# Optimization experiments

Hardware: AMD Instinct MI355X
Metric: run time of the kernel (lower is better)

The kernel has to match this reference:

```python
import jax, jax.numpy as jnp
import numpy as np

N_SERIES = 32768
N_TIME = 512
SEAS = 24
MAX_NUM_SERIES = 32768
OUTPUT_SIZE = 7


def setup_inputs() -> dict:
    key = jax.random.key(0)
    k1, k2, k3, k4, k5 = jax.random.split(key, 5)
    # y must be strictly positive (divisions and logs of levels)
    y = jax.random.uniform(k1, (N_SERIES, N_TIME), jnp.float32) + 0.5
    idxs = jax.random.randint(k2, (N_SERIES,), 0, MAX_NUM_SERIES)
    lev_sms = jax.random.normal(k3, (MAX_NUM_SERIES, 1), jnp.float32) * 0.5
    seas_sms = jax.random.normal(k4, (MAX_NUM_SERIES, 1), jnp.float32) * 0.5
    init_seas = jax.random.normal(k5, (MAX_NUM_SERIES, SEAS), jnp.float32) * 0.1
    return {
        "y": y,
        "idxs": idxs,
        "lev_sms": lev_sms,
        "seas_sms": seas_sms,
        "init_seas": init_seas,
        "seasonality": SEAS,
        "output_size": OUTPUT_SIZE,
    }


def _es_forward(y, idxs, lev_sms_p, seas_sms_p, init_seas_p, seasonality, output_size):
    n_series, n_time = y.shape
    lev_sms = jax.nn.sigmoid(lev_sms_p[idxs, 0])          # (n,)
    # NOTE: faithful to original code, which (buggy or not) derives seas_sms
    # from self.lev_sms as well; seas_sms_p is an unused parameter.
    seas_sms = jax.nn.sigmoid(lev_sms_p[idxs, 0])         # (n,)
    init_seas = jnp.exp(init_seas_p[idxs, :])             # (n, seasonality)

    lev0 = y[:, 0] / init_seas[:, 0]                      # levels[:,0]

    # Ring-buffer formulation of the lag-`seasonality` recurrence:
    # original reads seasonalities[:, t] and writes seasonalities[:, t+seasonality];
    # both map to slot t % seasonality (read-before-write). Initial buffer slots
    # equal init_seas columns (slot 0 = init_seas[:,0], which also covers the
    # duplicated entry seasonalities[:, seasonality]).
    positions = jnp.arange(1, n_time) % seasonality       # (n_time-1,)
    y_steps = y[:, 1:].T                                  # (n_time-1, n)

    def step(carry, xs):
        lev_prev, buf = carry                             # (n,), (n, seasonality)
        y_t, pos = xs
        seas_t = buf[:, pos]
        newlev = lev_sms * (y_t / seas_t) + (1.0 - lev_sms) * lev_prev
        newseason = seas_sms * (y_t / newlev) + (1.0 - seas_sms) * seas_t
        log_diff = jnp.log(newlev) - jnp.log(lev_prev)
        buf = buf.at[:, pos].set(newseason)
        return (newlev, buf), (newlev, newseason, log_diff)

    _, (levs, seasons, logd) = jax.lax.scan(step, (lev0, init_seas), (y_steps, positions))

    levels = jnp.concatenate([lev0[:, None], levs.T], axis=1)              # (n, n_time)
    seasonalities = jnp.concatenate(
        [init_seas, init_seas[:, :1], seasons.T], axis=1                   # (n, seasonality+n_time)
    )
    log_diff_of_levels = logd.T                                            # (n, n_time-1)

    if output_size > seasonality:
        # faithful to original (which uses len(seasonalities) == n_series)
        start = seasonalities.shape[0] - seasonality
        end = start + output_size - seasonality
        seasonalities = jnp.concatenate([seasonalities, seasonalities[:, start:end]], axis=1)

    return levels, seasonalities, log_diff_of_levels


def reference(y, idxs, lev_sms, seas_sms, init_seas, seasonality, output_size):
    return _es_forward(y, idxs, lev_sms, seas_sms, init_seas, seasonality, output_size)
```

## Files before the change

### kernel.cpp

```cpp
#include <hip/hip_runtime.h>

#define NT 512
#define SEASN 24

constexpr int SEA_STRIDE = NT + SEASN;
constexpr int LOG_STRIDE = NT - 1;
constexpr float LN2 = 0.6931471805599453f;

constexpr int YS = 65;
constexpr int TS = 33;

__device__ __forceinline__ float frcp(float x)  { return __builtin_amdgcn_rcpf(x); }
__device__ __forceinline__ float flog2(float x) { return __builtin_amdgcn_logf(x); }

__device__ __forceinline__ void gl_lds4(const float* g, float* lds) {
    __builtin_amdgcn_global_load_lds(
        (const __attribute__((address_space(1))) void*)g,
        (__attribute__((address_space(3))) void*)lds, 4, 0, 0);
}

template<int PHASE, bool FIRST>
__device__ __forceinline__ void compute_subtile(const float* __restrict__ yb,
                                                float* __restrict__ lt,
                                                float* __restrict__ st,
                                                float lsm, float (&buf)[SEASN],
                                                float& lev)
{
    float yp[32];
    #pragma unroll
    for (int k = 0; k < 32; ++k) yp[k] = yb[k];
    #pragma unroll
    for (int k = 0; k < 32; ++k) {
        const int pos = (PHASE + k) % SEASN;
        const float yt = yp[k];
        if (FIRST && k == 0) {
            lev = yt * frcp(buf[0]);
            lt[0] = lev;
            st[0] = buf[0];
        } else {
            const float sv = buf[pos];
            const float nl = lev + lsm * (yt * frcp(sv) - lev);
            const float ns = sv + lsm * (yt * frcp(nl) - sv);
            lt[k] = nl; st[k] = ns;
            lev = nl; buf[pos] = ns;
        }
    }
}

__device__ __forceinline__ void flush_sub(const float* __restrict__ lt,
                                          const float* __restrict__ st,
                                          int sf, int q, int rr, int sbase,
                                          float* __restrict__ levels,
                                          float* __restrict__ seasv,
                                          float* __restrict__ logd)
{
    const int tb = sf * 32;
    #pragma unroll
    for (int i = 0; i < 8; ++i) {
        const int r = 8 * i + rr;
        const size_t srow = (size_t)(sbase + r);
        const int off = r * TS + 4 * q;
        const float l0 = lt[off], l1 = lt[off+1], l2 = lt[off+2], l3 = lt[off+3];
        const float s0 = st[off], s1 = st[off+1], s2 = st[off+2], s3 = st[off+3];
        *(float4*)(levels + srow * NT + tb + 4*q)                  = make_float4(l0,l1,l2,l3);
        *(float4*)(seasv  + srow * SEA_STRIDE + SEASN + tb + 4*q)  = make_float4(s0,s1,s2,s3);
        const float lm1 = (q == 0) ? lt[r * TS + 32] : lt[off - 1];
        const float g0 = flog2(lm1), g1 = flog2(l0), g2 = flog2(l1),
                    g3 = flog2(l2),  g4 = flog2(l3);
        float* dp = logd + srow * LOG_STRIDE + tb + 4*q - 1;
        if (!(sf == 0 && q == 0)) dp[0] = (g1 - g0) * LN2;
        dp[1] = (g2 - g1) * LN2;
        dp[2] = (g3 - g2) * LN2;
        dp[3] = (g4 - g3) * LN2;
    }
}

__global__ __launch_bounds__(128)
void es_fwd(const float* __restrict__ y, const int* __restrict__ idxs,
            const float* __restrict__ lev_sms_p, const float* __restrict__ init_seas_p,
            float* __restrict__ levels, float* __restrict__ seasv,
            float* __restrict__ logd)
{
    __shared__ float ybuf[2][64 * YS];
    __shared__ float ltb [2][64 * TS];
    __shared__ float stb [2][64 * TS];

    const int tid   = threadIdx.x;
    const int wid   = tid >> 6;
    const int lane  = tid & 63;
    const int sbase = blockIdx.x * 64;
    const int q  = lane & 7;
    const int rr = lane >> 3;

    auto stage = [&](int T) {
        const float* g = y + (size_t)sbase * NT + T * 64 + lane;
        float* l = ybuf[T & 1];
        #pragma unroll
        for (int r = 0; r < 64; ++r)
            gl_lds4(g + (size_t)r * NT, l + r * YS);
    };

    float buf[SEASN];
    float lsm = 0.0f;
    float lev = 1.0f;

    if (wid == 0) {
        const int idx = idxs[sbase + lane];
        lsm = frcp(1.0f + __expf(-lev_sms_p[idx]));
        const float4* is4 = (const float4*)(init_seas_p + (size_t)idx * SEASN);
        #pragma unroll
        for (int g4i = 0; g4i < 6; ++g4i) {
            float4 v = is4[g4i];
            buf[4*g4i+0] = __expf(v.x); buf[4*g4i+1] = __expf(v.y);
            buf[4*g4i+2] = __expf(v.z); buf[4*g4i+3] = __expf(v.w);
        }
        #pragma unroll
        for (int j = 0; j < SEASN; ++j)
            ltb[1][lane * TS + j] = buf[j];
        asm volatile("s_waitcnt lgkmcnt(0)" ::: "memory");
    } else {
        stage(0);
        asm volatile("s_waitcnt vmcnt(0)" ::: "memory");
    }
    __builtin_amdgcn_s_barrier();
    asm volatile("" ::: "memory");

    for (int s = 0; s < 16; ++s) {
        if (wid == 0) {
            const float* yb = &ybuf[(s >> 1) & 1][lane * YS + (s & 1) * 32];
            float* lt = &ltb[s & 1][lane * TS];
            float* st = &stb[s & 1][lane * TS];
            lt[32] = lev;
            const int ph = s % 3;
            if (s == 0)       compute_subtile<0,  true >(yb, lt, st, lsm, buf, lev);
            else if (ph == 0) compute_subtile<0,  false>(yb, lt, st, lsm, buf, lev);
            else if (ph == 1) compute_subtile<8,  false>(yb, lt, st, lsm, buf, lev);
            else              compute_subtile<16, false>(yb, lt, st, lsm, buf, lev);
            asm volatile("s_waitcnt lgkmcnt(0)" ::: "memory");
        } else {
            const int T = (s >> 1) + 1;
            if (!(s & 1) && T < 8) stage(T);
            if (s == 0) {
                if (q < 6) {
                    #pragma unroll
                    for (int i = 0; i < 8; ++i) {
                        const int r = 8 * i + rr;
                        const int off = r * TS + 4 * q;
                        float4 v = make_float4(ltb[1][off],   ltb[1][off+1],
                                               ltb[1][off+2], ltb[1][off+3]);
                        *(float4*)(seasv + (size_t)(sbase + r) * SEA_STRIDE + 4 * q) = v;
                    }
                }
            } else {
                flush_sub(ltb[(s-1)&1], stb[(s-1)&1], s-1, q, rr, sbase,
                          levels, seasv, logd);
            }
            asm volatile("s_waitcnt vmcnt(48)" ::: "memory");
        }
        __builtin_amdgcn_s_barrier();
        asm volatile("" ::: "memory");
    }
    if (wid == 1)
        flush_sub(ltb[1], stb[1], 15, q, rr, sbase, levels, seasv, logd);
}

extern "C" void kernel_launch(void* const* d_in, const int* in_sizes, int n_in,
                              void* d_out, int out_size, void* d_ws, size_t ws_size,
                              hipStream_t stream)
{
    const float* y         = (const float*)d_in[0];
    const int*   idxs      = (const int*)d_in[1];
    const float* lev_sms   = (const float*)d_in[2];
    const float* init_seas = (const float*)d_in[4];
    const int n_series = in_sizes[1];

    float* levels = (float*)d_out;
    float* seasv  = levels + (size_t)n_series * NT;
    float* logdv  = seasv  + (size_t)n_series * SEA_STRIDE;

    es_fwd<<<n_series / 64, 128, 0, stream>>>(y, idxs, lev_sms, init_seas,
                                              levels, seasv, logdv);
}
```

Before: 329.3 us.

## Split y staging and output flushing across four producer/flusher wavefronts

Replaces the single helper wavefront, which staged all 64 rows of y and flushed all outputs, with four helper wavefronts that each handle 16 rows. The compute wavefront's sequential recurrence is unchanged. Spreading the loads, stores and log computations over more waves is meant to keep the helpers from being the bottleneck behind the compute wave. In exchange the block grows from 128 to 320 threads, which may lower occupancy, and the vmcnt waits are retuned for the smaller per-wave load count.

Result: faster. 309.3 us (-6.1%).

```diff
diff --git a/kernel.cpp b/kernel.cpp
--- a/kernel.cpp
+++ b/kernel.cpp
@@ -9,6 +9,7 @@
 
 constexpr int YS = 65;
 constexpr int TS = 33;
+constexpr int NF = 4;
 
 __device__ __forceinline__ float frcp(float x)  { return __builtin_amdgcn_rcpf(x); }
 __device__ __forceinline__ float flog2(float x) { return __builtin_amdgcn_logf(x); }
@@ -47,35 +48,7 @@
     }
 }
 
-__device__ __forceinline__ void flush_sub(const float* __restrict__ lt,
-                                          const float* __restrict__ st,
-                                          int sf, int q, int rr, int sbase,
-                                          float* __restrict__ levels,
-                                          float* __restrict__ seasv,
-                                          float* __restrict__ logd)
-{
-    const int tb = sf * 32;
-    #pragma unroll
-    for (int i = 0; i < 8; ++i) {
-        const int r = 8 * i + rr;
-        const size_t srow = (size_t)(sbase + r);
-        const int off = r * TS + 4 * q;
-        const float l0 = lt[off], l1 = lt[off+1], l2 = lt[off+2], l3 = lt[off+3];
-        const float s0 = st[off], s1 = st[off+1], s2 = st[off+2], s3 = st[off+3];
-        *(float4*)(levels + srow * NT + tb + 4*q)                  = make_float4(l0,l1,l2,l3);
-        *(float4*)(seasv  + srow * SEA_STRIDE + SEASN + tb + 4*q)  = make_float4(s0,s1,s2,s3);
-        const float lm1 = (q == 0) ? lt[r * TS + 32] : lt[off - 1];
-        const float g0 = flog2(lm1), g1 = flog2(l0), g2 = flog2(l1),
-                    g3 = flog2(l2),  g4 = flog2(l3);
-        float* dp = logd + srow * LOG_STRIDE + tb + 4*q - 1;
-        if (!(sf == 0 && q == 0)) dp[0] = (g1 - g0) * LN2;
-        dp[1] = (g2 - g1) * LN2;
-        dp[2] = (g3 - g2) * LN2;
-        dp[3] = (g4 - g3) * LN2;
-    }
-}
-
-__global__ __launch_bounds__(128)
+__global__ __launch_bounds__(64 * (NF + 1))
 void es_fwd(const float* __restrict__ y, const int* __restrict__ idxs,
             const float* __restrict__ lev_sms_p, const float* __restrict__ init_seas_p,
             float* __restrict__ levels, float* __restrict__ seasv,
@@ -89,44 +62,27 @@
     const int wid   = tid >> 6;
     const int lane  = tid & 63;
     const int sbase = blockIdx.x * 64;
-    const int q  = lane & 7;
-    const int rr = lane >> 3;
-
-    auto stage = [&](int T) {
-        const float* g = y + (size_t)sbase * NT + T * 64 + lane;
-        float* l = ybuf[T & 1];
-        #pragma unroll
-        for (int r = 0; r < 64; ++r)
-            gl_lds4(g + (size_t)r * NT, l + r * YS);
-    };
-
-    float buf[SEASN];
-    float lsm = 0.0f;
-    float lev = 1.0f;
 
     if (wid == 0) {
         const int idx = idxs[sbase + lane];
-        lsm = frcp(1.0f + __expf(-lev_sms_p[idx]));
+        const float lsm = frcp(1.0f + __expf(-lev_sms_p[idx]));
+        float buf[SEASN];
         const float4* is4 = (const float4*)(init_seas_p + (size_t)idx * SEASN);
         #pragma unroll
-        for (int g4i = 0; g4i < 6; ++g4i) {
-            float4 v = is4[g4i];
-            buf[4*g4i+0] = __expf(v.x); buf[4*g4i+1] = __expf(v.y);
-            buf[4*g4i+2] = __expf(v.z); buf[4*g4i+3] = __expf(v.w);
+        for (int g4 = 0; g4 < 6; ++g4) {
+            float4 v = is4[g4];
+            buf[4*g4+0] = __expf(v.x); buf[4*g4+1] = __expf(v.y);
+            buf[4*g4+2] = __expf(v.z); buf[4*g4+3] = __expf(v.w);
         }
         #pragma unroll
         for (int j = 0; j < SEASN; ++j)
             ltb[1][lane * TS + j] = buf[j];
         asm volatile("s_waitcnt lgkmcnt(0)" ::: "memory");
-    } else {
-        stage(0);
-        asm volatile("s_waitcnt vmcnt(0)" ::: "memory");
-    }
-    __builtin_amdgcn_s_barrier();
-    asm volatile("" ::: "memory");
+        __builtin_amdgcn_s_barrier();
+        asm volatile("" ::: "memory");
 
-    for (int s = 0; s < 16; ++s) {
-        if (wid == 0) {
+        float lev = 1.0f;
+        for (int s = 0; s < 16; ++s) {
             const float* yb = &ybuf[(s >> 1) & 1][lane * YS + (s & 1) * 32];
             float* lt = &ltb[s & 1][lane * TS];
             float* st = &stb[s & 1][lane * TS];
@@ -137,31 +93,79 @@
             else if (ph == 1) compute_subtile<8,  false>(yb, lt, st, lsm, buf, lev);
             else              compute_subtile<16, false>(yb, lt, st, lsm, buf, lev);
             asm volatile("s_waitcnt lgkmcnt(0)" ::: "memory");
-        } else {
-            const int T = (s >> 1) + 1;
-            if (!(s & 1) && T < 8) stage(T);
+            __builtin_amdgcn_s_barrier();
+            asm volatile("" ::: "memory");
+        }
+    } else {
+        const int f  = wid - 1;
+        const int q  = lane & 7;
+        const int rr = lane >> 3;
+        const int ra = 16 * f + rr;
+        const int rb = ra + 8;
+        const int offa = ra * TS + 4 * q;
+        const int offb = rb * TS + 4 * q;
+
+        auto stage = [&](int T) {
+            const float* g = y + (size_t)(sbase + 16 * f) * NT + T * 64 + lane;
+            float* l = &ybuf[T & 1][(16 * f) * YS];
+            #pragma unroll
+            for (int r = 0; r < 16; ++r)
+                gl_lds4(g + (size_t)r * NT, l + r * YS);
+        };
+
+        stage(0);
+        asm volatile("s_waitcnt vmcnt(0)" ::: "memory");
+        __builtin_amdgcn_s_barrier();
+        asm volatile("" ::: "memory");
+
+        float* lpa = levels + (size_t)(sbase + ra) * NT + 4 * q;
+        float* lpb = levels + (size_t)(sbase + rb) * NT + 4 * q;
+        float* spa = seasv  + (size_t)(sbase + ra) * SEA_STRIDE + SEASN + 4 * q;
+        float* spb = seasv  + (size_t)(sbase + rb) * SEA_STRIDE + SEASN + 4 * q;
+        float* dpa = logd   + (size_t)(sbase + ra) * LOG_STRIDE + 4 * q - 1;
+        float* dpb = logd   + (size_t)(sbase + rb) * LOG_STRIDE + 4 * q - 1;
+
+        auto flushrow = [&](const float* lt, const float* st, int off, int rX,
+                            float* lp, float* sp, float* dp, bool guard0) {
+            const float l0 = lt[off], l1 = lt[off+1], l2 = lt[off+2], l3 = lt[off+3];
+            const float s0 = st[off], s1 = st[off+1], s2 = st[off+2], s3 = st[off+3];
+            *(float4*)lp = make_float4(l0, l1, l2, l3);
+            *(float4*)sp = make_float4(s0, s1, s2, s3);
+            const float lm1 = (q == 0) ? lt[rX * TS + 32] : lt[off - 1];
+            const float g0 = flog2(lm1), g1 = flog2(l0), g2 = flog2(l1),
+                        g3 = flog2(l2),  g4 = flog2(l3);
+            if (!(guard0 && q == 0)) dp[0] = (g1 - g0) * LN2;
+            dp[1] = (g2 - g1) * LN2;
+            dp[2] = (g3 - g2) * LN2;
+            dp[3] = (g4 - g3) * LN2;
+        };
+
+        for (int s = 0; s < 16; ++s) {
             if (s == 0) {
                 if (q < 6) {
-                    #pragma unroll
-                    for (int i = 0; i < 8; ++i) {
-                        const int r = 8 * i + rr;
-                        const int off = r * TS + 4 * q;
-                        float4 v = make_float4(ltb[1][off],   ltb[1][off+1],
-                                               ltb[1][off+2], ltb[1][off+3]);
-                        *(float4*)(seasv + (size_t)(sbase + r) * SEA_STRIDE + 4 * q) = v;
-                    }
+                    float4 va = make_float4(ltb[1][offa],   ltb[1][offa+1],
+                                            ltb[1][offa+2], ltb[1][offa+3]);
+                    float4 vb = make_float4(ltb[1][offb],   ltb[1][offb+1],
+                                            ltb[1][offb+2], ltb[1][offb+3]);
+                    *(float4*)(seasv + (size_t)(sbase + ra) * SEA_STRIDE + 4 * q) = va;
+                    *(float4*)(seasv + (size_t)(sbase + rb) * SEA_STRIDE + 4 * q) = vb;
                 }
             } else {
-                flush_sub(ltb[(s-1)&1], stb[(s-1)&1], s-1, q, rr, sbase,
-                          levels, seasv, logd);
+                const float* lt = ltb[(s - 1) & 1];
+                const float* st = stb[(s - 1) & 1];
+                const bool guard0 = (s == 1);
+                flushrow(lt, st, offa, ra, lpa, spa, dpa, guard0);
+                flushrow(lt, st, offb, rb, lpb, spb, dpb, guard0);
+                lpa += 32; lpb += 32; spa += 32; spb += 32; dpa += 32; dpb += 32;
             }
-            asm volatile("s_waitcnt vmcnt(48)" ::: "memory");
+            if (!(s & 1) && s < 14) stage((s >> 1) + 1);
+            if (s & 1) asm volatile("s_waitcnt vmcnt(12)" ::: "memory");
+            __builtin_amdgcn_s_barrier();
+            asm volatile("" ::: "memory");
         }
-        __builtin_amdgcn_s_barrier();
-        asm volatile("" ::: "memory");
+        flushrow(ltb[1], stb[1], offa, ra, lpa, spa, dpa, false);
+        flushrow(ltb[1], stb[1], offb, rb, lpb, spb, dpb, false);
     }
-    if (wid == 1)
-        flush_sub(ltb[1], stb[1], 15, q, rr, sbase, levels, seasv, logd);
 }
 
 extern "C" void kernel_launch(void* const* d_in, const int* in_sizes, int n_in,
@@ -178,6 +182,6 @@
     float* seasv  = levels + (size_t)n_series * NT;
     float* logdv  = seasv  + (size_t)n_series * SEA_STRIDE;
 
-    es_fwd<<<n_series / 64, 128, 0, stream>>>(y, idxs, lev_sms, init_seas,
-                                              levels, seasv, logdv);
+    es_fwd<<<n_series / 64, 64 * (NF + 1), 0, stream>>>(y, idxs, lev_sms, init_seas,
+                                                        levels, seasv, logdv);
 }
```
